# Performance work log

Measured on AMD Instinct MI355X. Metric: run time of the kernel, lower is better.

The kernel has to match this reference:

```python
import jax, jax.numpy as jnp
import numpy as np

B, L, INP, HID, NCLS = 512, 256, 300, 256, 5  # trees, leaves/tree, embed dim, hidden, classes


def setup_inputs() -> dict:
    key = jax.random.key(0)
    ks = jax.random.split(key, 7)
    s_in = 1.0 / np.sqrt(INP).astype(np.float32)
    s_h = 1.0 / np.sqrt(HID).astype(np.float32)
    # W_leaf order: [inp_gate, out_gate, upd_gate]
    # W_nl order:  [inp_ln, inp_rn, fo_l_l, fo_l_r, fo_r_l, fo_r_r, out_ln, out_rn, upd_ln, upd_rn]
    return {
        "embeddings": jax.random.normal(ks[0], (B, L, INP), jnp.float32),
        "W_leaf": jax.random.uniform(ks[1], (3, INP, HID), jnp.float32, -s_in, s_in),
        "b_leaf": jax.random.uniform(ks[2], (3, HID), jnp.float32, -s_in, s_in),
        "W_nl": jax.random.uniform(ks[3], (10, HID, HID), jnp.float32, -s_h, s_h),
        "b_nl": jax.random.uniform(ks[4], (10, HID), jnp.float32, -s_h, s_h),
        "W_out": jax.random.uniform(ks[5], (HID, NCLS), jnp.float32, -s_h, s_h),
        "b_out": jax.random.uniform(ks[6], (NCLS,), jnp.float32, -s_h, s_h),
    }


def reference(embeddings, W_leaf, b_leaf, W_nl, b_nl, W_out, b_out):
    sig, tanh = jax.nn.sigmoid, jnp.tanh
    # ---- leaf nodes (depth 0), batched over all B*L leaves ----
    pre = jnp.einsum('bli,gih->blgh', embeddings, W_leaf) + b_leaf  # [B,L,3,H]
    i_g = sig(pre[:, :, 0])
    o_g = sig(pre[:, :, 1])
    u_g = tanh(pre[:, :, 2])
    c = i_g * u_g                      # [B,L,H]
    h = o_g * sig(c)                   # note: leaf uses sigmoid(cell), as in torch code
    logits = [jnp.einsum('bnh,hc->bnc', h, W_out) + b_out]
    # ---- internal nodes, level-synchronous ----
    Wl = W_nl[0::2]                    # [5,H,H] acting on left hidden
    Wr = W_nl[1::2]                    # [5,H,H] acting on right hidden
    bb = b_nl[0::2] + b_nl[1::2]       # [5,H]
    n = L
    while n > 1:
        lc, rc = c[:, 0::2], c[:, 1::2]
        lh, rh = h[:, 0::2], h[:, 1::2]
        pre = (jnp.einsum('bnh,ghk->bngk', lh, Wl)
               + jnp.einsum('bnh,ghk->bngk', rh, Wr) + bb)  # [B,n/2,5,H]
        inp_g = sig(pre[:, :, 0])
        fol_g = sig(pre[:, :, 1])
        for_g = sig(pre[:, :, 2])
        out_g = sig(pre[:, :, 3])
        upd_g = tanh(pre[:, :, 4])
        c = inp_g * upd_g + fol_g * lc + for_g * rc
        h = out_g * tanh(c)
        logits.append(jnp.einsum('bnh,hc->bnc', h, W_out) + b_out)
        n //= 2
    # per-node class scores for all 2L-1 nodes (leaves first, root last)
    return jnp.concatenate(logits, axis=1)  # [B, 2L-1, NCLS]
```

## Files before the change

### kernel.cpp

```cpp
#include <hip/hip_runtime.h>
#include <hip/hip_bf16.h>


#define HID 256

typedef __attribute__((ext_vector_type(8))) short short8;
typedef __attribute__((ext_vector_type(4))) float f32x4;
typedef __attribute__((ext_vector_type(4))) unsigned short ushort4v;

__device__ __forceinline__ float rcpf(float x) { return __builtin_amdgcn_rcpf(x); }
__device__ __forceinline__ float sigf(float x) { return rcpf(1.0f + __expf(-x)); }
__device__ __forceinline__ float tanhf_(float x) { return 2.0f * rcpf(1.0f + __expf(-2.0f * x)) - 1.0f; }
__device__ __forceinline__ float bf2f(unsigned short u) {
    union { unsigned int i; float f; } v; v.i = ((unsigned int)u) << 16; return v.f;
}
__device__ __forceinline__ unsigned short f2bf(float f) {
    __hip_bfloat16 b = __float2bfloat16(f);
    return *(unsigned short*)&b;
}
__device__ __forceinline__ void gload_lds16(const void* g, void* l) {
    __builtin_amdgcn_global_load_lds(
        (const __attribute__((address_space(1))) unsigned int*)g,
        (__attribute__((address_space(3))) unsigned int*)l, 16, 0, 0);
}

template <int NG, int K, bool LEAF>
__global__ __launch_bounds__(512, 1) void gemm_big8(
    const unsigned short* __restrict__ A,
    const unsigned short* __restrict__ BT,
    const float* __restrict__ bias,
    const float* __restrict__ cprev,
    float* __restrict__ cout,
    unsigned short* __restrict__ hout)
{
    constexpr int BN   = NG * 64;
    constexpr int NK   = K / 64;
    constexpr int NBW  = BN / 64;
    constexpr int BP0  = (NBW + 1) / 2;
    constexpr int ABUF = 256 * 128;
    constexpr int BBUF = BN * 128;
    constexpr int BUF  = ABUF + BBUF;

    __shared__ char smem[2 * BUF];

    const int t = threadIdx.x;
    const int lane = t & 63;
    const int w = t >> 6;
    const int wm = w >> 2, wn = w & 3;

    const int bid = blockIdx.x;
    const int xcd = bid & 7;
    const int slot = bid >> 3;
    const int cb = slot & 3;
    const int row0 = ((slot >> 2) * 8 + xcd) * 256;

    const int l3 = lane >> 3;
    const unsigned int swsrc = (unsigned int)(((lane & 7) ^ l3) * 16);
    unsigned int a_src[4];
    unsigned int b_src[NBW];
#pragma unroll
    for (int q = 0; q < 4; ++q)
        a_src[q] = (unsigned int)(row0 + (w * 4 + q) * 8 + l3) * (K * 2) + swsrc;
#pragma unroll
    for (int q = 0; q < NBW; ++q)
        b_src[q] = (unsigned int)(cb * BN + (w * NBW + q) * 8 + l3) * (K * 2) + swsrc;

    const int swz0 = ((lane >> 4) ^ (lane & 7)) * 16;
    const int swz1 = (((lane >> 4) + 4) ^ (lane & 7)) * 16;
    const int aoff = (wm * 128 + (lane & 15)) * 128;
    const int boff = (wn * (NG * 16) + (lane & 15)) * 128;

    f32x4 acc[8][NG] = {};
    short8 breg[NG][2];

    auto STAGE_A = [&](int buf, int kt, int half) {
        char* As = smem + buf * BUF;
        const unsigned int k0b = (unsigned int)kt * 128;
#pragma unroll
        for (int q = 2 * half; q < 2 * half + 2; ++q)
            gload_lds16((const char*)A + (size_t)(a_src[q] + k0b),
                        As + (w * 4 + q) * 1024);
    };
    auto STAGE_B = [&](int buf, int kt, int half) {
        char* Bs = smem + buf * BUF + ABUF;
        const unsigned int k0b = (unsigned int)kt * 128;
        const int q0 = half ? BP0 : 0;
        const int q1 = half ? NBW : BP0;
#pragma unroll
        for (int q = q0; q < q1; ++q)
            gload_lds16((const char*)BT + (size_t)(b_src[q] + k0b),
                        Bs + (w * NBW + q) * 1024);
    };

#define PHASE(MFB, STAGE_STMT, FINAL)                                         \
    {                                                                          \
        short8 a0k0 = *(const short8*)(As + aoff + (MFB) * 2048 + swz0);       \
        short8 a0k1 = *(const short8*)(As + aoff + (MFB) * 2048 + swz1);       \
        short8 a1k0 = *(const short8*)(As + aoff + (MFB + 1) * 2048 + swz0);   \
        short8 a1k1 = *(const short8*)(As + aoff + (MFB + 1) * 2048 + swz1);   \
        STAGE_STMT;                                                            \
        asm volatile("" ::: "memory");                                         \
        __builtin_amdgcn_s_barrier();                                          \
        asm volatile("" ::: "memory");                                         \
        __builtin_amdgcn_s_setprio(1);                                         \
        _Pragma("unroll")                                                      \
        for (int g = 0; g < NG; ++g) {                                         \
            acc[MFB][g] = __builtin_amdgcn_mfma_f32_16x16x32_bf16(             \
                a0k0, breg[g][0], acc[MFB][g], 0, 0, 0);                       \
            acc[MFB + 1][g] = __builtin_amdgcn_mfma_f32_16x16x32_bf16(         \
                a1k0, breg[g][0], acc[MFB + 1][g], 0, 0, 0);                   \
            acc[MFB][g] = __builtin_amdgcn_mfma_f32_16x16x32_bf16(             \
                a0k1, breg[g][1], acc[MFB][g], 0, 0, 0);                       \
            acc[MFB + 1][g] = __builtin_amdgcn_mfma_f32_16x16x32_bf16(         \
                a1k1, breg[g][1], acc[MFB + 1][g], 0, 0, 0);                   \
        }                                                                      \
        __builtin_amdgcn_s_setprio(0);                                         \
        if (FINAL) {                                                           \
            asm volatile("s_waitcnt lgkmcnt(0)" ::: "memory");                  \
            __builtin_amdgcn_sched_barrier(0);                                  \
        }                                                                      \
        asm volatile("" ::: "memory");                                         \
        __builtin_amdgcn_s_barrier();                                          \
        asm volatile("" ::: "memory");                                         \
    }

    STAGE_A(0, 0, 0); STAGE_A(0, 0, 1);
    STAGE_B(0, 0, 0); STAGE_B(0, 0, 1);

    for (int kt = 0; kt < NK; ++kt) {
        const int cur = kt & 1;
        const char* As = smem + cur * BUF;
        const char* Bs = As + ABUF;
        const bool pf = (kt + 1) < NK;

        asm volatile("s_waitcnt vmcnt(0)" ::: "memory");
        __builtin_amdgcn_s_barrier();
        asm volatile("" ::: "memory");

#pragma unroll
        for (int g = 0; g < NG; ++g) {
            breg[g][0] = *(const short8*)(Bs + boff + g * 2048 + swz0);
            breg[g][1] = *(const short8*)(Bs + boff + g * 2048 + swz1);
        }
        PHASE(0, if (pf) STAGE_A(cur ^ 1, kt + 1, 0), false)
        PHASE(2, if (pf) STAGE_A(cur ^ 1, kt + 1, 1), false)
        PHASE(4, if (pf) STAGE_B(cur ^ 1, kt + 1, 0), false)
        PHASE(6, if (pf) STAGE_B(cur ^ 1, kt + 1, 1), true)
    }
#undef PHASE

    const int cl = wn * 16 + (lane & 15);
    const int c = cb * 64 + cl;
#pragma unroll
    for (int mf = 0; mf < 8; ++mf) {
#pragma unroll
        for (int j = 0; j < 4; ++j) {
            const int r = row0 + wm * 128 + mf * 16 + ((lane >> 4) << 2) + j;
            float cv, hv;
            if constexpr (LEAF) {
                float p0 = acc[mf][0][j] + bias[c];
                float p1 = acc[mf][1][j] + bias[256 + c];
                float p2 = acc[mf][2][j] + bias[512 + c];
                cv = sigf(p0) * tanhf_(p2);
                hv = sigf(p1) * sigf(cv);
            } else {
                float p0 = acc[mf][0][j] + bias[c];
                float p1 = acc[mf][1][j] + bias[256 + c];
                float p2 = acc[mf][2][j] + bias[512 + c];
                float p3 = acc[mf][3][j] + bias[768 + c];
                float p4 = acc[mf][4][j] + bias[1024 + c];
                float lc = cprev[(size_t)r * 512 + c];
                float rc = cprev[(size_t)r * 512 + 256 + c];
                cv = sigf(p0) * tanhf_(p4) + sigf(p1) * lc + sigf(p2) * rc;
                hv = sigf(p3) * tanhf_(cv);
            }
            cout[(size_t)r * 256 + c] = cv;
            hout[(size_t)r * 256 + c] = f2bf(hv);
        }
    }
}

template <int NG, int K>
__global__ __launch_bounds__(256, 3) void gemm_small(
    const unsigned short* __restrict__ A,
    const unsigned short* __restrict__ BT,
    const float* __restrict__ bias,
    const float* __restrict__ cprev,
    float* __restrict__ cout,
    unsigned short* __restrict__ hout)
{
    constexpr int CS  = 32;
    constexpr int BN  = NG * CS;
    constexpr int NK  = K / 64;
    constexpr int NBW = BN / 32;
    constexpr int ABUF = 128 * 128;

    __shared__ char smem[2 * ABUF + BN * 128];
    char* Bs = smem + 2 * ABUF;

    const int t = threadIdx.x;
    const int lane = t & 63;
    const int w = t >> 6;
    const int wm = w >> 1, wn = w & 1;
    const int cb = blockIdx.x;
    const int row0 = blockIdx.y * 128;

    const int l3 = lane >> 3;
    const unsigned int swsrc = (unsigned int)(((lane & 7) ^ l3) * 16);
    unsigned int a_src[4];
    unsigned int b_src[NBW];
#pragma unroll
    for (int q = 0; q < 4; ++q)
        a_src[q] = (unsigned int)(row0 + (w * 4 + q) * 8 + l3) * (K * 2) + swsrc;
#pragma unroll
    for (int q = 0; q < NBW; ++q)
        b_src[q] = (unsigned int)(cb * BN + (w * NBW + q) * 8 + l3) * (K * 2) + swsrc;

    const int swz0 = ((lane >> 4) ^ (lane & 7)) * 16;
    const int swz1 = (((lane >> 4) + 4) ^ (lane & 7)) * 16;
    const int aoff = (wm * 64 + (lane & 15)) * 128;
    const int boff = (wn * 16 + (lane & 15)) * 128;

    f32x4 acc[4][NG] = {};

    auto STAGE_A = [&](int buf, int kt) {
        char* As = smem + buf * ABUF;
        const unsigned int k0b = (unsigned int)kt * 128;
#pragma unroll
        for (int q = 0; q < 4; ++q)
            gload_lds16((const char*)A + (size_t)(a_src[q] + k0b),
                        As + (w * 4 + q) * 1024);
    };
    auto STAGE_B = [&](int kt) {
        const unsigned int k0b = (unsigned int)kt * 128;
#pragma unroll
        for (int q = 0; q < NBW; ++q)
            gload_lds16((const char*)BT + (size_t)(b_src[q] + k0b),
                        Bs + (w * NBW + q) * 1024);
    };

    STAGE_A(0, 0);
    STAGE_B(0);
    asm volatile("s_waitcnt vmcnt(0)" ::: "memory");
    __builtin_amdgcn_s_barrier();
    asm volatile("" ::: "memory");

#pragma unroll
    for (int kt = 0; kt < NK; ++kt) {
        const int cur = kt & 1;
        if (kt + 1 < NK) STAGE_A(cur ^ 1, kt + 1);
        const char* As = smem + cur * ABUF;
#pragma unroll
        for (int ks = 0; ks < 2; ++ks) {
            const int sw = ks ? swz1 : swz0;
            short8 a[4];
#pragma unroll
            for (int mf = 0; mf < 4; ++mf)
                a[mf] = *(const short8*)(As + aoff + mf * 2048 + sw);
#pragma unroll
            for (int g = 0; g < NG; ++g) {
                short8 b = *(const short8*)(Bs + g * (CS * 128) + boff + sw);
#pragma unroll
                for (int mf = 0; mf < 4; ++mf)
                    acc[mf][g] = __builtin_amdgcn_mfma_f32_16x16x32_bf16(
                        a[mf], b, acc[mf][g], 0, 0, 0);
            }
        }
        asm volatile("" ::: "memory");
        __builtin_amdgcn_s_barrier();
        asm volatile("" ::: "memory");
        if (kt + 1 < NK) {
            STAGE_B(kt + 1);
            asm volatile("s_waitcnt vmcnt(0)" ::: "memory");
        }
        __builtin_amdgcn_s_barrier();
        asm volatile("" ::: "memory");
    }

#pragma unroll
    for (int mf = 0; mf < 4; ++mf) {
#pragma unroll
        for (int j = 0; j < 4; ++j) {
            const int r = row0 + wm * 64 + mf * 16 + ((lane >> 4) << 2) + j;
            const int cl = wn * 16 + (lane & 15);
            const int c = cb * 32 + cl;
            float p0 = acc[mf][0][j] + bias[c];
            float p1 = acc[mf][1][j] + bias[256 + c];
            float p2 = acc[mf][2][j] + bias[512 + c];
            float p3 = acc[mf][3][j] + bias[768 + c];
            float p4 = acc[mf][4][j] + bias[1024 + c];
            float lc = cprev[(size_t)r * 512 + c];
            float rc = cprev[(size_t)r * 512 + 256 + c];
            float cv = sigf(p0) * tanhf_(p4) + sigf(p1) * lc + sigf(p2) * rc;
            float hv = sigf(p3) * tanhf_(cv);
            cout[(size_t)r * 256 + c] = cv;
            hout[(size_t)r * 256 + c] = f2bf(hv);
        }
    }
}

__global__ __launch_bounds__(256) void logits_all(
    const unsigned short* __restrict__ hA,
    const unsigned short* __restrict__ hRest,
    const float* __restrict__ W_out, const float* __restrict__ b_out,
    float* __restrict__ out)
{
    const int t = threadIdx.x;
    const int part = t & 15;
    const int rl = t >> 4;

    float wreg[80];
#pragma unroll
    for (int e = 0; e < 16; ++e)
#pragma unroll
        for (int cls = 0; cls < 5; ++cls)
            wreg[e * 5 + cls] = W_out[(part * 16 + e) * 5 + cls];
    const float b0 = b_out[0], b1 = b_out[1], b2 = b_out[2],
                b3 = b_out[3], b4 = b_out[4];

    for (int ch = blockIdx.x; ch < 16352; ch += gridDim.x) {
        const int R = ch * 16 + rl;
        const unsigned short* h = (R < 131072)
            ? hA + (size_t)R * HID
            : hRest + (size_t)(R - 131072) * HID;

        short8 h0 = *(const short8*)(h + part * 16);
        short8 h1 = *(const short8*)(h + part * 16 + 8);
        float a0 = 0.f, a1 = 0.f, a2 = 0.f, a3 = 0.f, a4 = 0.f;
#pragma unroll
        for (int e = 0; e < 8; ++e) {
            float f = bf2f((unsigned short)h0[e]);
            a0 = fmaf(f, wreg[e * 5 + 0], a0);
            a1 = fmaf(f, wreg[e * 5 + 1], a1);
            a2 = fmaf(f, wreg[e * 5 + 2], a2);
            a3 = fmaf(f, wreg[e * 5 + 3], a3);
            a4 = fmaf(f, wreg[e * 5 + 4], a4);
        }
#pragma unroll
        for (int e = 0; e < 8; ++e) {
            float f = bf2f((unsigned short)h1[e]);
            a0 = fmaf(f, wreg[(8 + e) * 5 + 0], a0);
            a1 = fmaf(f, wreg[(8 + e) * 5 + 1], a1);
            a2 = fmaf(f, wreg[(8 + e) * 5 + 2], a2);
            a3 = fmaf(f, wreg[(8 + e) * 5 + 3], a3);
            a4 = fmaf(f, wreg[(8 + e) * 5 + 4], a4);
        }
#pragma unroll
        for (int m = 8; m >= 1; m >>= 1) {
            a0 += __shfl_xor(a0, m);
            a1 += __shfl_xor(a1, m);
            a2 += __shfl_xor(a2, m);
            a3 += __shfl_xor(a3, m);
            a4 += __shfl_xor(a4, m);
        }
        if (part == 0) {
            unsigned int V = 262144u - (unsigned int)R;
            int lev = 17 - (31 - __clz(V - 1));
            int start = 262144 - (1 << (18 - lev));
            int local = R - start;
            int nb = 8 - lev;
            int b = local >> nb, j = local & ((1 << nb) - 1);
            int off = 512 - (1 << (9 - lev));
            size_t o = ((size_t)b * 511 + off + j) * 5;
            out[o + 0] = a0 + b0;
            out[o + 1] = a1 + b1;
            out[o + 2] = a2 + b2;
            out[o + 3] = a3 + b3;
            out[o + 4] = a4 + b4;
        }
    }
}

__global__ __launch_bounds__(256) void prep_weights(
    const float* __restrict__ W_leaf, const float* __restrict__ W_nl,
    const float* __restrict__ b_nl,
    unsigned short* __restrict__ BleafT,
    unsigned short* __restrict__ BlevTn,
    unsigned short* __restrict__ BlevTo,
    float* __restrict__ bb)
{
    const int T1 = 768 * 320, T2 = 1280 * 512, T3 = 1280 * 512, T4 = 5 * 256;
    for (int idx = blockIdx.x * 256 + threadIdx.x; idx < T1 + T2 + T3 + T4;
         idx += gridDim.x * 256) {
        if (idx < T1) {
            int colp = idx / 320, k = idx % 320;
            int cbv = colp / 192, r = colp % 192;
            int wn = r / 48, r2 = r % 48;
            int g = r2 >> 4, cl = r2 & 15;
            int c = cbv * 64 + wn * 16 + cl;
            float v = (k < 300) ? W_leaf[((size_t)g * 300 + k) * 256 + c] : 0.0f;
            BleafT[(size_t)colp * 320 + k] = f2bf(v);
        } else if (idx < T1 + T2) {
            int i2 = idx - T1;
            int colp = i2 / 512, k = i2 % 512;
            int cbv = colp / 320, r = colp % 320;
            int wn = r / 80, r2 = r % 80;
            int g = r2 >> 4, cl = r2 & 15;
            int c = cbv * 64 + wn * 16 + cl;
            float v = W_nl[((size_t)(2 * g + (k >= 256)) * 256 + (k & 255)) * 256 + c];
            BlevTn[(size_t)colp * 512 + k] = f2bf(v);
        } else if (idx < T1 + T2 + T3) {
            int i2 = idx - T1 - T2;
            int colp = i2 / 512, k = i2 % 512;
            int cb8 = colp / 160, r = colp % 160;
            int g = r >> 5, cl = r & 31;
            int c = cb8 * 32 + cl;
            float v = W_nl[((size_t)(2 * g + (k >= 256)) * 256 + (k & 255)) * 256 + c];
            BlevTo[(size_t)colp * 512 + k] = f2bf(v);
        } else {
            int i3 = idx - T1 - T2 - T3;
            bb[i3] = b_nl[(size_t)(i3 >> 8) * 512 + (i3 & 255)] +
                     b_nl[(size_t)(i3 >> 8) * 512 + 256 + (i3 & 255)];
        }
    }
}

__global__ __launch_bounds__(256) void emb_to_bf16(
    const float* __restrict__ emb, unsigned short* __restrict__ embB)
{
    const int total = 131072 * 80;
    for (int idx = blockIdx.x * 256 + threadIdx.x; idx < total;
         idx += gridDim.x * 256) {
        int r = idx / 80, q = idx % 80;
        ushort4v o;
        if (q < 75) {
            const float4 v = *(const float4*)(emb + (size_t)r * 300 + q * 4);
            o.x = f2bf(v.x); o.y = f2bf(v.y); o.z = f2bf(v.z); o.w = f2bf(v.w);
        } else {
            o.x = 0; o.y = 0; o.z = 0; o.w = 0;
        }
        *(ushort4v*)(embB + (size_t)r * 320 + q * 4) = o;
    }
}

extern "C" void kernel_launch(void* const* d_in, const int* in_sizes, int n_in,
                              void* d_out, int out_size, void* d_ws, size_t ws_size,
                              hipStream_t stream) {
    const float* emb    = (const float*)d_in[0];
    const float* W_leaf = (const float*)d_in[1];
    const float* b_leaf = (const float*)d_in[2];
    const float* W_nl   = (const float*)d_in[3];
    const float* b_nl   = (const float*)d_in[4];
    const float* W_out  = (const float*)d_in[5];
    const float* b_out  = (const float*)d_in[6];
    float* out = (float*)d_out;

    char* ws = (char*)d_ws;
    unsigned short* embB   = (unsigned short*)(ws);
    unsigned short* hRest  = (unsigned short*)(ws);
    unsigned short* BleafT = (unsigned short*)(ws + 83886080);
    unsigned short* BlevTn = (unsigned short*)(ws + 84377600);
    unsigned short* BlevTo = (unsigned short*)(ws + 85688320);
    float*          bb     = (float*)(ws + 86999040);
    float*          cA     = (float*)(ws + 87004160);
    unsigned short* hA     = (unsigned short*)(ws + 221221888);
    float*          cB     = (float*)(ws + 288330752);

    prep_weights<<<1024, 256, 0, stream>>>(W_leaf, W_nl, b_nl,
                                           BleafT, BlevTn, BlevTo, bb);
    emb_to_bf16<<<2048, 256, 0, stream>>>(emb, embB);

    gemm_big8<3, 320, true><<<2048, 512, 0, stream>>>(
        embB, BleafT, b_leaf, nullptr, cA, hA);

    const unsigned short* hp = hA;
    const float* cp = cA;
    size_t hoff = 0;
    for (int lev = 1; lev <= 8; ++lev) {
        int n = 1 << (8 - lev);
        int M = 512 * n;
        float* cd = (lev & 1) ? cB : cA;
        unsigned short* hd = hRest + hoff;
        if (M >= 16384) {
            gemm_big8<5, 512, false><<<(M / 256) * 4, 512, 0, stream>>>(
                hp, BlevTn, bb, cp, cd, hd);
        } else {
            gemm_small<5, 512><<<dim3(8, M / 128), 256, 0, stream>>>(
                hp, BlevTo, bb, cp, cd, hd);
        }
        cp = cd;
        hp = hd;
        hoff += (size_t)M * HID;
    }

    logits_all<<<2048, 256, 0, stream>>>(hA, hRest, W_out, b_out, out);
}
```

Baseline: 470.1 us.

## Replace LDS-staged big-tile GEMM with register-direct MFMA GEMM and smaller tiles

The double-buffered LDS pipeline (256xBN block tiles, 8 waves, barriers and global_load_lds staging) is replaced by a simpler kernel. Each wave loads A and B fragments straight from global memory into registers and issues MFMAs, with 256-thread blocks covering 256 rows by 16 columns per gate group and occupancy hint 2. The weight prep layout changes to match the new 16-column slices. This removes LDS traffic and barrier overhead but drops cross-wave data reuse, so the same A rows are re-read by 16 column-slice blocks and global/L2 traffic rises.

```diff
diff --git a/kernel.cpp b/kernel.cpp
--- a/kernel.cpp
+++ b/kernel.cpp
@@ -25,7 +25,7 @@
 }
 
 template <int NG, int K, bool LEAF>
-__global__ __launch_bounds__(512, 1) void gemm_big8(
+__global__ __launch_bounds__(256, 2) void gemm_reg(
     const unsigned short* __restrict__ A,
     const unsigned short* __restrict__ BT,
     const float* __restrict__ bias,
@@ -33,129 +33,52 @@
     float* __restrict__ cout,
     unsigned short* __restrict__ hout)
 {
-    constexpr int BN   = NG * 64;
-    constexpr int NK   = K / 64;
-    constexpr int NBW  = BN / 64;
-    constexpr int BP0  = (NBW + 1) / 2;
-    constexpr int ABUF = 256 * 128;
-    constexpr int BBUF = BN * 128;
-    constexpr int BUF  = ABUF + BBUF;
-
-    __shared__ char smem[2 * BUF];
-
     const int t = threadIdx.x;
     const int lane = t & 63;
     const int w = t >> 6;
-    const int wm = w >> 2, wn = w & 3;
+    const int lr = lane & 15, lk = lane >> 4;
 
     const int bid = blockIdx.x;
     const int xcd = bid & 7;
     const int slot = bid >> 3;
-    const int cb = slot & 3;
-    const int row0 = ((slot >> 2) * 8 + xcd) * 256;
-
-    const int l3 = lane >> 3;
-    const unsigned int swsrc = (unsigned int)(((lane & 7) ^ l3) * 16);
-    unsigned int a_src[4];
-    unsigned int b_src[NBW];
-#pragma unroll
-    for (int q = 0; q < 4; ++q)
-        a_src[q] = (unsigned int)(row0 + (w * 4 + q) * 8 + l3) * (K * 2) + swsrc;
-#pragma unroll
-    for (int q = 0; q < NBW; ++q)
-        b_src[q] = (unsigned int)(cb * BN + (w * NBW + q) * 8 + l3) * (K * 2) + swsrc;
-
-    const int swz0 = ((lane >> 4) ^ (lane & 7)) * 16;
-    const int swz1 = (((lane >> 4) + 4) ^ (lane & 7)) * 16;
-    const int aoff = (wm * 128 + (lane & 15)) * 128;
-    const int boff = (wn * (NG * 16) + (lane & 15)) * 128;
-
-    f32x4 acc[8][NG] = {};
-    short8 breg[NG][2];
-
-    auto STAGE_A = [&](int buf, int kt, int half) {
-        char* As = smem + buf * BUF;
-        const unsigned int k0b = (unsigned int)kt * 128;
-#pragma unroll
-        for (int q = 2 * half; q < 2 * half + 2; ++q)
-            gload_lds16((const char*)A + (size_t)(a_src[q] + k0b),
-                        As + (w * 4 + q) * 1024);
-    };
-    auto STAGE_B = [&](int buf, int kt, int half) {
-        char* Bs = smem + buf * BUF + ABUF;
-        const unsigned int k0b = (unsigned int)kt * 128;
-        const int q0 = half ? BP0 : 0;
-        const int q1 = half ? NBW : BP0;
-#pragma unroll
-        for (int q = q0; q < q1; ++q)
-            gload_lds16((const char*)BT + (size_t)(b_src[q] + k0b),
-                        Bs + (w * NBW + q) * 1024);
-    };
-
-#define PHASE(MFB, STAGE_STMT, FINAL)                                         \
-    {                                                                          \
-        short8 a0k0 = *(const short8*)(As + aoff + (MFB) * 2048 + swz0);       \
-        short8 a0k1 = *(const short8*)(As + aoff + (MFB) * 2048 + swz1);       \
-        short8 a1k0 = *(const short8*)(As + aoff + (MFB + 1) * 2048 + swz0);   \
-        short8 a1k1 = *(const short8*)(As + aoff + (MFB + 1) * 2048 + swz1);   \
-        STAGE_STMT;                                                            \
-        asm volatile("" ::: "memory");                                         \
-        __builtin_amdgcn_s_barrier();                                          \
-        asm volatile("" ::: "memory");                                         \
-        __builtin_amdgcn_s_setprio(1);                                         \
-        _Pragma("unroll")                                                      \
-        for (int g = 0; g < NG; ++g) {                                         \
-            acc[MFB][g] = __builtin_amdgcn_mfma_f32_16x16x32_bf16(             \
-                a0k0, breg[g][0], acc[MFB][g], 0, 0, 0);                       \
-            acc[MFB + 1][g] = __builtin_amdgcn_mfma_f32_16x16x32_bf16(         \
-                a1k0, breg[g][0], acc[MFB + 1][g], 0, 0, 0);                   \
-            acc[MFB][g] = __builtin_amdgcn_mfma_f32_16x16x32_bf16(             \
-                a0k1, breg[g][1], acc[MFB][g], 0, 0, 0);                       \
-            acc[MFB + 1][g] = __builtin_amdgcn_mfma_f32_16x16x32_bf16(         \
-                a1k1, breg[g][1], acc[MFB + 1][g], 0, 0, 0);                   \
-        }                                                                      \
-        __builtin_amdgcn_s_setprio(0);                                         \
-        if (FINAL) {                                                           \
-            asm volatile("s_waitcnt lgkmcnt(0)" ::: "memory");                  \
-            __builtin_amdgcn_sched_barrier(0);                                  \
-        }                                                                      \
-        asm volatile("" ::: "memory");                                         \
-        __builtin_amdgcn_s_barrier();                                          \
-        asm volatile("" ::: "memory");                                         \
-    }
-
-    STAGE_A(0, 0, 0); STAGE_A(0, 0, 1);
-    STAGE_B(0, 0, 0); STAGE_B(0, 0, 1);
-
-    for (int kt = 0; kt < NK; ++kt) {
-        const int cur = kt & 1;
-        const char* As = smem + cur * BUF;
-        const char* Bs = As + ABUF;
-        const bool pf = (kt + 1) < NK;
-
-        asm volatile("s_waitcnt vmcnt(0)" ::: "memory");
-        __builtin_amdgcn_s_barrier();
-        asm volatile("" ::: "memory");
-
-#pragma unroll
-        for (int g = 0; g < NG; ++g) {
-            breg[g][0] = *(const short8*)(Bs + boff + g * 2048 + swz0);
-            breg[g][1] = *(const short8*)(Bs + boff + g * 2048 + swz1);
-        }
-        PHASE(0, if (pf) STAGE_A(cur ^ 1, kt + 1, 0), false)
-        PHASE(2, if (pf) STAGE_A(cur ^ 1, kt + 1, 1), false)
-        PHASE(4, if (pf) STAGE_B(cur ^ 1, kt + 1, 0), false)
-        PHASE(6, if (pf) STAGE_B(cur ^ 1, kt + 1, 1), true)
-    }
-#undef PHASE
-
-    const int cl = wn * 16 + (lane & 15);
-    const int c = cb * 64 + cl;
-#pragma unroll
-    for (int mf = 0; mf < 8; ++mf) {
+    const int sl = slot & 15;
+    const int rowblk = (slot >> 4) * 8 + xcd;
+    const int wrow0 = rowblk * 256 + w * 64;
+
+    const unsigned short* aP[4];
+#pragma unroll
+    for (int mf = 0; mf < 4; ++mf)
+        aP[mf] = A + (size_t)(wrow0 + mf * 16 + lr) * K + lk * 8;
+    const unsigned short* bP[NG];
+#pragma unroll
+    for (int g = 0; g < NG; ++g)
+        bP[g] = BT + (size_t)(sl * NG * 16 + g * 16 + lr) * K + lk * 8;
+
+    f32x4 acc[4][NG] = {};
+
+#pragma unroll 2
+    for (int ks = 0; ks < K / 32; ++ks) {
+        short8 a[4], b[NG];
+#pragma unroll
+        for (int mf = 0; mf < 4; ++mf)
+            a[mf] = *(const short8*)(aP[mf] + ks * 32);
+#pragma unroll
+        for (int g = 0; g < NG; ++g)
+            b[g] = *(const short8*)(bP[g] + ks * 32);
+#pragma unroll
+        for (int g = 0; g < NG; ++g)
+#pragma unroll
+            for (int mf = 0; mf < 4; ++mf)
+                acc[mf][g] = __builtin_amdgcn_mfma_f32_16x16x32_bf16(
+                    a[mf], b[g], acc[mf][g], 0, 0, 0);
+    }
+
+    const int c = sl * 16 + lr;
+#pragma unroll
+    for (int mf = 0; mf < 4; ++mf) {
 #pragma unroll
         for (int j = 0; j < 4; ++j) {
-            const int r = row0 + wm * 128 + mf * 16 + ((lane >> 4) << 2) + j;
+            const int r = wrow0 + mf * 16 + lk * 4 + j;
             float cv, hv;
             if constexpr (LEAF) {
                 float p0 = acc[mf][0][j] + bias[c];
@@ -384,19 +307,17 @@
          idx += gridDim.x * 256) {
         if (idx < T1) {
             int colp = idx / 320, k = idx % 320;
-            int cbv = colp / 192, r = colp % 192;
-            int wn = r / 48, r2 = r % 48;
-            int g = r2 >> 4, cl = r2 & 15;
-            int c = cbv * 64 + wn * 16 + cl;
+            int sl = colp / 48, r = colp % 48;
+            int g = r >> 4, cl = r & 15;
+            int c = sl * 16 + cl;
             float v = (k < 300) ? W_leaf[((size_t)g * 300 + k) * 256 + c] : 0.0f;
             BleafT[(size_t)colp * 320 + k] = f2bf(v);
         } else if (idx < T1 + T2) {
             int i2 = idx - T1;
             int colp = i2 / 512, k = i2 % 512;
-            int cbv = colp / 320, r = colp % 320;
-            int wn = r / 80, r2 = r % 80;
-            int g = r2 >> 4, cl = r2 & 15;
-            int c = cbv * 64 + wn * 16 + cl;
+            int sl = colp / 80, r = colp % 80;
+            int g = r >> 4, cl = r & 15;
+            int c = sl * 16 + cl;
             float v = W_nl[((size_t)(2 * g + (k >= 256)) * 256 + (k & 255)) * 256 + c];
             BlevTn[(size_t)colp * 512 + k] = f2bf(v);
         } else if (idx < T1 + T2 + T3) {
@@ -460,7 +381,7 @@
                                            BleafT, BlevTn, BlevTo, bb);
     emb_to_bf16<<<2048, 256, 0, stream>>>(emb, embB);
 
-    gemm_big8<3, 320, true><<<2048, 512, 0, stream>>>(
+    gemm_reg<3, 320, true><<<8192, 256, 0, stream>>>(
         embB, BleafT, b_leaf, nullptr, cA, hA);
 
     const unsigned short* hp = hA;
@@ -472,7 +393,7 @@
         float* cd = (lev & 1) ? cB : cA;
         unsigned short* hd = hRest + hoff;
         if (M >= 16384) {
-            gemm_big8<5, 512, false><<<(M / 256) * 4, 512, 0, stream>>>(
+            gemm_reg<5, 512, false><<<M / 16, 256, 0, stream>>>(
                 hp, BlevTn, bb, cp, cd, hd);
         } else {
             gemm_small<5, 512><<<dim3(8, M / 128), 256, 0, stream>>>(
```

Result: slower. 935.2 us (+99.0%).
